# Performance work log

Hardware: AMD Instinct MI355X
Metric: run time of the kernel (lower is better)

The kernel has to match this reference:

```python
import jax, jax.numpy as jnp
import numpy as np

N_NODES = 100000
N_EDGES = 2500000
IN_CH = 32
HID = 16
OUT_CH = 32


def setup_inputs() -> dict:
    key = jax.random.key(0)
    ks = jax.random.split(key, 10)
    x = jax.random.normal(ks[0], (N_NODES, IN_CH), dtype=jnp.float32)
    edge_index = jax.random.randint(ks[1], (2, N_EDGES), 0, N_NODES, dtype=jnp.int64)
    # conv1 MLP: Linear(in,16) -> ReLU -> Linear(16,out)
    W1 = jax.random.normal(ks[2], (IN_CH, HID), dtype=jnp.float32) / np.sqrt(IN_CH)
    b1 = jnp.zeros((HID,), dtype=jnp.float32)
    W2 = jax.random.normal(ks[3], (HID, OUT_CH), dtype=jnp.float32) / np.sqrt(HID)
    b2 = jnp.zeros((OUT_CH,), dtype=jnp.float32)
    # conv2 MLP: Linear(out,16) -> ReLU -> Linear(16,out)
    W3 = jax.random.normal(ks[4], (OUT_CH, HID), dtype=jnp.float32) / np.sqrt(OUT_CH)
    b3 = jnp.zeros((HID,), dtype=jnp.float32)
    W4 = jax.random.normal(ks[5], (HID, OUT_CH), dtype=jnp.float32) / np.sqrt(HID)
    b4 = jnp.zeros((OUT_CH,), dtype=jnp.float32)
    return {"x": x, "edge_index": edge_index, "W1": W1, "b1": b1, "W2": W2,
            "b2": b2, "W3": W3, "b3": b3, "W4": W4, "b4": b4}


def _gin_conv(x, src, dst, W_a, b_a, W_b, b_b):
    # GINConv (eps=0): nn((1+eps)*x + sum_{j in N(i)} x_j)
    agg = jax.ops.segment_sum(x[src], dst, num_segments=x.shape[0])  # [N, d]
    h = x + agg
    h = jnp.maximum(h @ W_a + b_a, 0.0)  # Linear -> ReLU
    return h @ W_b + b_b                 # Linear


def reference(x, edge_index, W1, b1, W2, b2, W3, b3, W4, b4):
    src, dst = edge_index[0], edge_index[1]
    h = _gin_conv(x, src, dst, W1, b1, W2, b2)
    h = jnp.maximum(h, 0.0)  # F.relu between convs
    out = _gin_conv(h, src, dst, W3, b3, W4, b4)
    return out
```

## Files before the change

### kernel.cpp

```cpp
#include <hip/hip_runtime.h>

typedef unsigned short ushort_t;
typedef unsigned int uint_t;

#define BKT_SHIFT 8
#define BKT_NODES 256
#define NBKT_MAX 400
#define EPB 8192
#define SCOL_CAP 8192
#define NPB 32
#define SCOL_N 1536

__device__ __forceinline__ ushort_t f2bf(float f) {
    unsigned u = __float_as_uint(f);
    unsigned r = (u + 0x7FFFu + ((u >> 16) & 1u)) >> 16;
    return (ushort_t)r;
}
__device__ __forceinline__ float bflo(uint_t u) { return __uint_as_float(u << 16); }
__device__ __forceinline__ float bfhi(uint_t u) { return __uint_as_float(u & 0xFFFF0000u); }

__global__ void to_bf16(const float4* __restrict__ in, ushort_t* __restrict__ out, int n4) {
    int i = blockIdx.x * blockDim.x + threadIdx.x;
    if (i < n4) {
        float4 v = in[i];
        out[i * 4 + 0] = f2bf(v.x);
        out[i * 4 + 1] = f2bf(v.y);
        out[i * 4 + 2] = f2bf(v.z);
        out[i * 4 + 3] = f2bf(v.w);
    }
}


__global__ void histA(const int* __restrict__ dst, int* __restrict__ hist,
                      int E, int NBKT) {
    __shared__ int lcnt[NBKT_MAX];
    int t = threadIdx.x, blk = blockIdx.x;
    for (int b = t; b < NBKT; b += 512) lcnt[b] = 0;
    __syncthreads();
    int e0 = blk * EPB;
    #pragma unroll
    for (int i = 0; i < 16; ++i) {
        int e = e0 + i * 512 + t;
        if (e < E) atomicAdd(&lcnt[dst[e] >> BKT_SHIFT], 1);
    }
    __syncthreads();
    for (int b = t; b < NBKT; b += 512) hist[blk * NBKT + b] = lcnt[b];
}

__global__ void colscan(int* __restrict__ hist, int* __restrict__ T,
                        int NBLK, int NBKT) {
    __shared__ int lds[256];
    int b = blockIdx.x, t = threadIdx.x;
    int j0 = t * 4;
    int v0 = (j0 + 0 < NBLK) ? hist[(j0 + 0) * NBKT + b] : 0;
    int v1 = (j0 + 1 < NBLK) ? hist[(j0 + 1) * NBKT + b] : 0;
    int v2 = (j0 + 2 < NBLK) ? hist[(j0 + 2) * NBKT + b] : 0;
    int v3 = (j0 + 3 < NBLK) ? hist[(j0 + 3) * NBKT + b] : 0;
    lds[t] = v0 + v1 + v2 + v3;
    __syncthreads();
    for (int off = 1; off < 256; off <<= 1) {
        int add = (t >= off) ? lds[t - off] : 0;
        __syncthreads();
        lds[t] += add;
        __syncthreads();
    }
    int p = (t == 0) ? 0 : lds[t - 1];
    if (j0 + 0 < NBLK) hist[(j0 + 0) * NBKT + b] = p;  p += v0;
    if (j0 + 1 < NBLK) hist[(j0 + 1) * NBKT + b] = p;  p += v1;
    if (j0 + 2 < NBLK) hist[(j0 + 2) * NBKT + b] = p;  p += v2;
    if (j0 + 3 < NBLK) hist[(j0 + 3) * NBKT + b] = p;
    if (t == 255) T[b] = lds[255];
}

__global__ void scan_small(const int* __restrict__ in, int* __restrict__ out,
                           int M, int E) {
    __shared__ int lds[1024];
    int t = threadIdx.x;
    int base = t * 4;
    int v0 = (base + 0 < M) ? in[base + 0] : 0;
    int v1 = (base + 1 < M) ? in[base + 1] : 0;
    int v2 = (base + 2 < M) ? in[base + 2] : 0;
    int v3 = (base + 3 < M) ? in[base + 3] : 0;
    lds[t] = v0 + v1 + v2 + v3;
    __syncthreads();
    for (int off = 1; off < 1024; off <<= 1) {
        int add = (t >= off) ? lds[t - off] : 0;
        __syncthreads();
        lds[t] += add;
        __syncthreads();
    }
    int p = (t == 0) ? 0 : lds[t - 1];
    if (base + 0 < M) out[base + 0] = p;  p += v0;
    if (base + 1 < M) out[base + 1] = p;  p += v1;
    if (base + 2 < M) out[base + 2] = p;  p += v2;
    if (base + 3 < M) out[base + 3] = p;
    if (t == 0) out[M] = E;
}

__global__ void scatter_kernel(const int* __restrict__ src, const int* __restrict__ dst,
                               const int* __restrict__ hist, const int* __restrict__ Tscan,
                               int* __restrict__ staged, int E, int NBKT) {
    __shared__ int lbase[NBKT_MAX];
    __shared__ int lcur[NBKT_MAX];
    int t = threadIdx.x, blk = blockIdx.x;
    for (int b = t; b < NBKT; b += 512) {
        lbase[b] = hist[blk * NBKT + b] + Tscan[b];
        lcur[b] = 0;
    }
    __syncthreads();
    int e0 = blk * EPB;
    #pragma unroll
    for (int i = 0; i < 16; ++i) {
        int e = e0 + i * 512 + t;
        if (e < E) {
            int d = dst[e], s = src[e];
            int b = d >> BKT_SHIFT;
            int r = atomicAdd(&lcur[b], 1);
            staged[lbase[b] + r] = ((d & (BKT_NODES - 1)) << 24) | s;
        }
    }
}

__global__ void fine_fill(const int* __restrict__ staged, const int* __restrict__ Tscan,
                          int* __restrict__ rp, int* __restrict__ col,
                          int N, int E, int NBKT, int q1, int q2, int q3) {
    __shared__ int scnt[1024];
    __shared__ int srel[1024];
    __shared__ int scur[1024];
    __shared__ int swsum[256];
    __shared__ int scol[SCOL_CAP];
    int b = blockIdx.x, t = threadIdx.x;
    int n0 = b << BKT_SHIFT;
    int nn = min(BKT_NODES, N - n0);
    int e0 = Tscan[b];
    int e1 = Tscan[b + 1];
    int m = e1 - e0;

    #pragma unroll
    for (int j = 0; j < 4; ++j) { scnt[t * 4 + j] = 0; scur[t * 4 + j] = 0; }
    __syncthreads();
    for (int i = t; i < m; i += 256) {
        int v = staged[e0 + i];
        int dl = ((unsigned)v) >> 24;
        int s = v & 0xFFFFFF;
        int q = (s >= q2) ? ((s >= q3) ? 3 : 2) : ((s >= q1) ? 1 : 0);
        atomicAdd(&scnt[dl * 4 + q], 1);
    }
    __syncthreads();
    int c0 = scnt[t * 4 + 0], c1 = scnt[t * 4 + 1];
    int c2 = scnt[t * 4 + 2], c3 = scnt[t * 4 + 3];
    int tot = c0 + c1 + c2 + c3;
    swsum[t] = tot;
    __syncthreads();
    for (int off = 1; off < 256; off <<= 1) {
        int add = (t >= off) ? swsum[t - off] : 0;
        __syncthreads();
        swsum[t] += add;
        __syncthreads();
    }
    int excl = swsum[t] - tot;
    srel[t * 4 + 0] = excl;
    srel[t * 4 + 1] = excl + c0;
    srel[t * 4 + 2] = excl + c0 + c1;
    srel[t * 4 + 3] = excl + c0 + c1 + c2;
    if (t < nn) rp[n0 + t] = e0 + excl;
    if (b == NBKT - 1 && t == 0) rp[N] = E;
    __syncthreads();

    if (m <= SCOL_CAP) {
        for (int i = t; i < m; i += 256) {
            int v = staged[e0 + i];
            int dl = ((unsigned)v) >> 24;
            int s = v & 0xFFFFFF;
            int q = (s >= q2) ? ((s >= q3) ? 3 : 2) : ((s >= q1) ? 1 : 0);
            int p = srel[dl * 4 + q] + atomicAdd(&scur[dl * 4 + q], 1);
            scol[p] = s;
        }
        __syncthreads();
        for (int i = t; i < m; i += 256) col[e0 + i] = scol[i];
    } else {
        for (int i = t; i < m; i += 256) {
            int v = staged[e0 + i];
            int dl = ((unsigned)v) >> 24;
            int s = v & 0xFFFFFF;
            int q = (s >= q2) ? ((s >= q3) ? 3 : 2) : ((s >= q1) ? 1 : 0);
            int p = srel[dl * 4 + q] + atomicAdd(&scur[dl * 4 + q], 1);
            col[e0 + p] = s;
        }
    }
}


template <bool RELU_OUT, bool OUT_BF16>
__global__ void agg_mlp(const ushort_t* __restrict__ xin, const int* __restrict__ rp,
                        const int* __restrict__ col,
                        const float* __restrict__ Wa, const float* __restrict__ ba,
                        const float* __restrict__ Wb, const float* __restrict__ bb,
                        void* __restrict__ outv, int N) {
    __shared__ float sWa[32 * 16];
    __shared__ float sWb[16 * 32];
    __shared__ float sba[16], sbb[32];
    __shared__ float sv[NPB * 33];
    __shared__ float st1[NPB * 17];
    __shared__ int scol[SCOL_N];

    int t = threadIdx.x;
    sWa[t] = Wa[t];  sWa[t + 256] = Wa[t + 256];
    sWb[t] = Wb[t];  sWb[t + 256] = Wb[t + 256];
    if (t < 16) sba[t] = ba[t];
    if (t < 32) sbb[t] = bb[t];

    int base = blockIdx.x * NPB;
    int kb = rp[base];
    int kt = rp[min(base + NPB, N)];
    int tot = kt - kb;
    bool ovf = (tot > SCOL_N);
    if (!ovf) {
        for (int i = t; i < tot; i += 256)
            scol[i] = __builtin_nontemporal_load(col + kb + i);
    }
    __syncthreads();

    int ln = t >> 3;
    int sl = t & 7;
    int n  = base + ln;
    bool act = (n < N);
    const uint2* x2 = (const uint2*)xin;

    if (act) {
        uint2 us = x2[(size_t)n * 8 + sl];
        float v0 = bflo(us.x), v1 = bfhi(us.x), v2 = bflo(us.y), v3 = bfhi(us.y);
        int ks = rp[n], ke = rp[n + 1];
        if (!ovf) {
            int k = ks - kb, kend = ke - kb;
            for (; k + 8 <= kend; k += 8) {
                int s0 = scol[k + 0], s1 = scol[k + 1], s2 = scol[k + 2], s3 = scol[k + 3];
                int s4 = scol[k + 4], s5 = scol[k + 5], s6 = scol[k + 6], s7 = scol[k + 7];
                uint2 u0 = x2[(size_t)s0 * 8 + sl];
                uint2 u1 = x2[(size_t)s1 * 8 + sl];
                uint2 u2 = x2[(size_t)s2 * 8 + sl];
                uint2 u3 = x2[(size_t)s3 * 8 + sl];
                uint2 u4 = x2[(size_t)s4 * 8 + sl];
                uint2 u5 = x2[(size_t)s5 * 8 + sl];
                uint2 u6 = x2[(size_t)s6 * 8 + sl];
                uint2 u7 = x2[(size_t)s7 * 8 + sl];
                v0 += ((bflo(u0.x) + bflo(u1.x)) + (bflo(u2.x) + bflo(u3.x)))
                    + ((bflo(u4.x) + bflo(u5.x)) + (bflo(u6.x) + bflo(u7.x)));
                v1 += ((bfhi(u0.x) + bfhi(u1.x)) + (bfhi(u2.x) + bfhi(u3.x)))
                    + ((bfhi(u4.x) + bfhi(u5.x)) + (bfhi(u6.x) + bfhi(u7.x)));
                v2 += ((bflo(u0.y) + bflo(u1.y)) + (bflo(u2.y) + bflo(u3.y)))
                    + ((bflo(u4.y) + bflo(u5.y)) + (bflo(u6.y) + bflo(u7.y)));
                v3 += ((bfhi(u0.y) + bfhi(u1.y)) + (bfhi(u2.y) + bfhi(u3.y)))
                    + ((bfhi(u4.y) + bfhi(u5.y)) + (bfhi(u6.y) + bfhi(u7.y)));
            }
            for (; k < kend; ++k) {
                uint2 u = x2[(size_t)scol[k] * 8 + sl];
                v0 += bflo(u.x); v1 += bfhi(u.x); v2 += bflo(u.y); v3 += bfhi(u.y);
            }
        } else {
            for (int k = ks; k < ke; ++k) {
                uint2 u = x2[(size_t)col[k] * 8 + sl];
                v0 += bflo(u.x); v1 += bfhi(u.x); v2 += bflo(u.y); v3 += bfhi(u.y);
            }
        }
        int c0 = sl * 4;
        sv[ln * 33 + c0 + 0] = v0; sv[ln * 33 + c0 + 1] = v1;
        sv[ln * 33 + c0 + 2] = v2; sv[ln * 33 + c0 + 3] = v3;
    }
    __syncthreads();

    if (act) {
        float ha = sba[sl], hb = sba[sl + 8];
        #pragma unroll
        for (int cc = 0; cc < 32; ++cc) {
            float vc = sv[ln * 33 + cc];
            ha += vc * sWa[cc * 16 + sl];
            hb += vc * sWa[cc * 16 + sl + 8];
        }
        st1[ln * 17 + sl]     = fmaxf(ha, 0.f);
        st1[ln * 17 + sl + 8] = fmaxf(hb, 0.f);
    }
    __syncthreads();

    if (act) {
        int c0 = sl * 4;
        float a0 = sbb[c0], a1 = sbb[c0 + 1], a2 = sbb[c0 + 2], a3 = sbb[c0 + 3];
        #pragma unroll
        for (int j = 0; j < 16; ++j) {
            float hj = st1[ln * 17 + j];
            a0 += hj * sWb[j * 32 + c0];
            a1 += hj * sWb[j * 32 + c0 + 1];
            a2 += hj * sWb[j * 32 + c0 + 2];
            a3 += hj * sWb[j * 32 + c0 + 3];
        }
        if (RELU_OUT) {
            a0 = fmaxf(a0, 0.f); a1 = fmaxf(a1, 0.f);
            a2 = fmaxf(a2, 0.f); a3 = fmaxf(a3, 0.f);
        }
        if (OUT_BF16) {
            uint_t p0 = (uint_t)f2bf(a0) | ((uint_t)f2bf(a1) << 16);
            uint_t p1 = (uint_t)f2bf(a2) | ((uint_t)f2bf(a3) << 16);
            uint_t* o = (uint_t*)outv + (size_t)n * 16 + sl * 2;
            __builtin_nontemporal_store(p0, o);
            __builtin_nontemporal_store(p1, o + 1);
        } else {
            float* o = (float*)outv + (size_t)n * 32 + c0;
            __builtin_nontemporal_store(a0, o);
            __builtin_nontemporal_store(a1, o + 1);
            __builtin_nontemporal_store(a2, o + 2);
            __builtin_nontemporal_store(a3, o + 3);
        }
    }
}


extern "C" void kernel_launch(void* const* d_in, const int* in_sizes, int n_in,
                              void* d_out, int out_size, void* d_ws, size_t ws_size,
                              hipStream_t stream) {
    const float* x  = (const float*)d_in[0];
    const int*   ei = (const int*)d_in[1];
    const float* W1 = (const float*)d_in[2];
    const float* b1 = (const float*)d_in[3];
    const float* W2 = (const float*)d_in[4];
    const float* b2 = (const float*)d_in[5];
    const float* W3 = (const float*)d_in[6];
    const float* b3 = (const float*)d_in[7];
    const float* W4 = (const float*)d_in[8];
    const float* b4 = (const float*)d_in[9];

    const int N = in_sizes[0] / 32;
    const int E = in_sizes[1] / 2;
    const int* src = ei;
    const int* dst = ei + E;

    const int NBKT = (N + BKT_NODES - 1) >> BKT_SHIFT;
    const int NBLK = (E + EPB - 1) / EPB;

    char* ws = (char*)d_ws;
    size_t o = 0;
    auto alloc = [&](size_t bytes) -> char* {
        o = (o + 255) & ~(size_t)255;
        char* r = ws + o;
        o += bytes;
        return r;
    };
    int*      hist   = (int*)     alloc(4 * (size_t)NBLK * NBKT);
    int*      T      = (int*)     alloc(4 * (size_t)NBKT);
    int*      Tscan  = (int*)     alloc(4 * (size_t)(NBKT + 1));
    int*      staged = (int*)     alloc(4 * (size_t)E);
    int*      rp     = (int*)     alloc(4 * (size_t)(N + 1));
    int*      col    = (int*)     alloc(4 * (size_t)E);
    ushort_t* xb     = (ushort_t*)alloc(2 * (size_t)N * 32);
    ushort_t* hb     = (ushort_t*)alloc(2 * (size_t)N * 32);

    int n4 = N * 32 / 4;
    to_bf16<<<(n4 + 255) / 256, 256, 0, stream>>>((const float4*)x, xb, n4);

    histA<<<NBLK, 512, 0, stream>>>(dst, hist, E, NBKT);
    colscan<<<NBKT, 256, 0, stream>>>(hist, T, NBLK, NBKT);
    scan_small<<<1, 1024, 0, stream>>>(T, Tscan, NBKT, E);
    scatter_kernel<<<NBLK, 512, 0, stream>>>(src, dst, hist, Tscan, staged, E, NBKT);
    int q1 = N / 4, q2 = N / 2, q3 = (3 * N) / 4;
    fine_fill<<<NBKT, 256, 0, stream>>>(staged, Tscan, rp, col, N, E, NBKT, q1, q2, q3);

    agg_mlp<true,  true ><<<(N + NPB - 1) / NPB, 256, 0, stream>>>(xb, rp, col,
                                                                   W1, b1, W2, b2, hb, N);
    agg_mlp<false, false><<<(N + NPB - 1) / NPB, 256, 0, stream>>>(hb, rp, col,
                                                                   W3, b3, W4, b4, d_out, N);
}
```

Measured before the change: 205.2 us.

## Apply first linear before aggregation to gather 16-wide features instead of 32

```diff
diff --git a/kernel.cpp b/kernel.cpp
--- a/kernel.cpp
+++ b/kernel.cpp
@@ -8,8 +8,8 @@
 #define NBKT_MAX 400
 #define EPB 8192
 #define SCOL_CAP 8192
-#define NPB 32
-#define SCOL_N 1536
+#define NPB16 64
+#define SCOL_N16 2560
 
 __device__ __forceinline__ ushort_t f2bf(float f) {
     unsigned u = __float_as_uint(f);
@@ -19,15 +19,39 @@
 __device__ __forceinline__ float bflo(uint_t u) { return __uint_as_float(u << 16); }
 __device__ __forceinline__ float bfhi(uint_t u) { return __uint_as_float(u & 0xFFFF0000u); }
 
-__global__ void to_bf16(const float4* __restrict__ in, ushort_t* __restrict__ out, int n4) {
-    int i = blockIdx.x * blockDim.x + threadIdx.x;
-    if (i < n4) {
-        float4 v = in[i];
-        out[i * 4 + 0] = f2bf(v.x);
-        out[i * 4 + 1] = f2bf(v.y);
-        out[i * 4 + 2] = f2bf(v.z);
-        out[i * 4 + 3] = f2bf(v.w);
-    }
+__global__ void lin_in(const float4* __restrict__ x4, const float* __restrict__ W,
+                       ushort_t* __restrict__ z, int N) {
+    __shared__ float sW[32 * 16];
+    int t = threadIdx.x;
+    sW[t] = W[t];
+    sW[t + 256] = W[t + 256];
+    __syncthreads();
+    int n = blockIdx.x * 256 + t;
+    if (n >= N) return;
+    float acc[16];
+    #pragma unroll
+    for (int c = 0; c < 16; ++c) acc[c] = 0.f;
+    const float4* xr = x4 + (size_t)n * 8;
+    #pragma unroll
+    for (int k4 = 0; k4 < 8; ++k4) {
+        float4 xv = xr[k4];
+        #pragma unroll
+        for (int c = 0; c < 16; ++c) {
+            acc[c] += xv.x * sW[(k4 * 4 + 0) * 16 + c];
+            acc[c] += xv.y * sW[(k4 * 4 + 1) * 16 + c];
+            acc[c] += xv.z * sW[(k4 * 4 + 2) * 16 + c];
+            acc[c] += xv.w * sW[(k4 * 4 + 3) * 16 + c];
+        }
+    }
+    uint_t w[8];
+    #pragma unroll
+    for (int i = 0; i < 8; ++i)
+        w[i] = (uint_t)f2bf(acc[2 * i]) | ((uint_t)f2bf(acc[2 * i + 1]) << 16);
+    uint4* zo = (uint4*)(z + (size_t)n * 16);
+    uint4 a; a.x = w[0]; a.y = w[1]; a.z = w[2]; a.w = w[3];
+    uint4 b; b.x = w[4]; b.y = w[5]; b.z = w[6]; b.w = w[7];
+    zo[0] = a;
+    zo[1] = b;
 }
 
 
@@ -191,44 +215,45 @@
 }
 
 
-template <bool RELU_OUT, bool OUT_BF16>
-__global__ void agg_mlp(const ushort_t* __restrict__ xin, const int* __restrict__ rp,
-                        const int* __restrict__ col,
-                        const float* __restrict__ Wa, const float* __restrict__ ba,
-                        const float* __restrict__ Wb, const float* __restrict__ bb,
-                        void* __restrict__ outv, int N) {
-    __shared__ float sWa[32 * 16];
+template <bool CHAIN>
+__global__ void agg_mlp16(const ushort_t* __restrict__ zin, const int* __restrict__ rp,
+                          const int* __restrict__ col,
+                          const float* __restrict__ ba,
+                          const float* __restrict__ Wb, const float* __restrict__ bb,
+                          const float* __restrict__ Wc,
+                          void* __restrict__ outv, int N) {
     __shared__ float sWb[16 * 32];
+    __shared__ float sWc[32 * 16];
     __shared__ float sba[16], sbb[32];
-    __shared__ float sv[NPB * 33];
-    __shared__ float st1[NPB * 17];
-    __shared__ int scol[SCOL_N];
+    __shared__ float sh[NPB16 * 17];
+    __shared__ float sr[NPB16 * 33];
+    __shared__ int scol[SCOL_N16];
 
     int t = threadIdx.x;
-    sWa[t] = Wa[t];  sWa[t + 256] = Wa[t + 256];
     sWb[t] = Wb[t];  sWb[t + 256] = Wb[t + 256];
+    if (CHAIN) { sWc[t] = Wc[t];  sWc[t + 256] = Wc[t + 256]; }
     if (t < 16) sba[t] = ba[t];
     if (t < 32) sbb[t] = bb[t];
 
-    int base = blockIdx.x * NPB;
+    int base = blockIdx.x * NPB16;
     int kb = rp[base];
-    int kt = rp[min(base + NPB, N)];
+    int kt = rp[min(base + NPB16, N)];
     int tot = kt - kb;
-    bool ovf = (tot > SCOL_N);
+    bool ovf = (tot > SCOL_N16);
     if (!ovf) {
         for (int i = t; i < tot; i += 256)
             scol[i] = __builtin_nontemporal_load(col + kb + i);
     }
     __syncthreads();
 
-    int ln = t >> 3;
-    int sl = t & 7;
+    int ln = t >> 2;
+    int sl = t & 3;
     int n  = base + ln;
     bool act = (n < N);
-    const uint2* x2 = (const uint2*)xin;
+    const uint2* zp = (const uint2*)zin;
 
     if (act) {
-        uint2 us = x2[(size_t)n * 8 + sl];
+        uint2 us = zp[(size_t)n * 4 + sl];
         float v0 = bflo(us.x), v1 = bfhi(us.x), v2 = bflo(us.y), v3 = bfhi(us.y);
         int ks = rp[n], ke = rp[n + 1];
         if (!ovf) {
@@ -236,14 +261,14 @@
             for (; k + 8 <= kend; k += 8) {
                 int s0 = scol[k + 0], s1 = scol[k + 1], s2 = scol[k + 2], s3 = scol[k + 3];
                 int s4 = scol[k + 4], s5 = scol[k + 5], s6 = scol[k + 6], s7 = scol[k + 7];
-                uint2 u0 = x2[(size_t)s0 * 8 + sl];
-                uint2 u1 = x2[(size_t)s1 * 8 + sl];
-                uint2 u2 = x2[(size_t)s2 * 8 + sl];
-                uint2 u3 = x2[(size_t)s3 * 8 + sl];
-                uint2 u4 = x2[(size_t)s4 * 8 + sl];
-                uint2 u5 = x2[(size_t)s5 * 8 + sl];
-                uint2 u6 = x2[(size_t)s6 * 8 + sl];
-                uint2 u7 = x2[(size_t)s7 * 8 + sl];
+                uint2 u0 = zp[(size_t)s0 * 4 + sl];
+                uint2 u1 = zp[(size_t)s1 * 4 + sl];
+                uint2 u2 = zp[(size_t)s2 * 4 + sl];
+                uint2 u3 = zp[(size_t)s3 * 4 + sl];
+                uint2 u4 = zp[(size_t)s4 * 4 + sl];
+                uint2 u5 = zp[(size_t)s5 * 4 + sl];
+                uint2 u6 = zp[(size_t)s6 * 4 + sl];
+                uint2 u7 = zp[(size_t)s7 * 4 + sl];
                 v0 += ((bflo(u0.x) + bflo(u1.x)) + (bflo(u2.x) + bflo(u3.x)))
                     + ((bflo(u4.x) + bflo(u5.x)) + (bflo(u6.x) + bflo(u7.x)));
                 v1 += ((bfhi(u0.x) + bfhi(u1.x)) + (bfhi(u2.x) + bfhi(u3.x)))
@@ -254,61 +279,64 @@
                     + ((bfhi(u4.y) + bfhi(u5.y)) + (bfhi(u6.y) + bfhi(u7.y)));
             }
             for (; k < kend; ++k) {
-                uint2 u = x2[(size_t)scol[k] * 8 + sl];
+                uint2 u = zp[(size_t)scol[k] * 4 + sl];
                 v0 += bflo(u.x); v1 += bfhi(u.x); v2 += bflo(u.y); v3 += bfhi(u.y);
             }
         } else {
             for (int k = ks; k < ke; ++k) {
-                uint2 u = x2[(size_t)col[k] * 8 + sl];
+                uint2 u = zp[(size_t)col[k] * 4 + sl];
                 v0 += bflo(u.x); v1 += bfhi(u.x); v2 += bflo(u.y); v3 += bfhi(u.y);
             }
         }
         int c0 = sl * 4;
-        sv[ln * 33 + c0 + 0] = v0; sv[ln * 33 + c0 + 1] = v1;
-        sv[ln * 33 + c0 + 2] = v2; sv[ln * 33 + c0 + 3] = v3;
+        sh[ln * 17 + c0 + 0] = fmaxf(v0 + sba[c0 + 0], 0.f);
+        sh[ln * 17 + c0 + 1] = fmaxf(v1 + sba[c0 + 1], 0.f);
+        sh[ln * 17 + c0 + 2] = fmaxf(v2 + sba[c0 + 2], 0.f);
+        sh[ln * 17 + c0 + 3] = fmaxf(v3 + sba[c0 + 3], 0.f);
     }
     __syncthreads();
 
     if (act) {
-        float ha = sba[sl], hb = sba[sl + 8];
+        int c0 = sl * 8;
+        float o[8];
         #pragma unroll
-        for (int cc = 0; cc < 32; ++cc) {
-            float vc = sv[ln * 33 + cc];
-            ha += vc * sWa[cc * 16 + sl];
-            hb += vc * sWa[cc * 16 + sl + 8];
-        }
-        st1[ln * 17 + sl]     = fmaxf(ha, 0.f);
-        st1[ln * 17 + sl + 8] = fmaxf(hb, 0.f);
-    }
-    __syncthreads();
-
-    if (act) {
-        int c0 = sl * 4;
-        float a0 = sbb[c0], a1 = sbb[c0 + 1], a2 = sbb[c0 + 2], a3 = sbb[c0 + 3];
+        for (int j = 0; j < 8; ++j) o[j] = sbb[c0 + j];
         #pragma unroll
         for (int j = 0; j < 16; ++j) {
-            float hj = st1[ln * 17 + j];
-            a0 += hj * sWb[j * 32 + c0];
-            a1 += hj * sWb[j * 32 + c0 + 1];
-            a2 += hj * sWb[j * 32 + c0 + 2];
-            a3 += hj * sWb[j * 32 + c0 + 3];
-        }
-        if (RELU_OUT) {
-            a0 = fmaxf(a0, 0.f); a1 = fmaxf(a1, 0.f);
-            a2 = fmaxf(a2, 0.f); a3 = fmaxf(a3, 0.f);
-        }
-        if (OUT_BF16) {
+            float hj = sh[ln * 17 + j];
+            #pragma unroll
+            for (int cc = 0; cc < 8; ++cc)
+                o[cc] += hj * sWb[j * 32 + c0 + cc];
+        }
+        if (CHAIN) {
+            #pragma unroll
+            for (int cc = 0; cc < 8; ++cc)
+                sr[ln * 33 + c0 + cc] = fmaxf(o[cc], 0.f);
+        } else {
+            float* op = (float*)outv + (size_t)n * 32 + c0;
+            #pragma unroll
+            for (int cc = 0; cc < 8; ++cc)
+                __builtin_nontemporal_store(o[cc], op + cc);
+        }
+    }
+    if (CHAIN) {
+        __syncthreads();
+        if (act) {
+            int c0 = sl * 4;
+            float a0 = 0.f, a1 = 0.f, a2 = 0.f, a3 = 0.f;
+            #pragma unroll
+            for (int j = 0; j < 32; ++j) {
+                float rj = sr[ln * 33 + j];
+                a0 += rj * sWc[j * 16 + c0 + 0];
+                a1 += rj * sWc[j * 16 + c0 + 1];
+                a2 += rj * sWc[j * 16 + c0 + 2];
+                a3 += rj * sWc[j * 16 + c0 + 3];
+            }
             uint_t p0 = (uint_t)f2bf(a0) | ((uint_t)f2bf(a1) << 16);
             uint_t p1 = (uint_t)f2bf(a2) | ((uint_t)f2bf(a3) << 16);
-            uint_t* o = (uint_t*)outv + (size_t)n * 16 + sl * 2;
-            __builtin_nontemporal_store(p0, o);
-            __builtin_nontemporal_store(p1, o + 1);
-        } else {
-            float* o = (float*)outv + (size_t)n * 32 + c0;
-            __builtin_nontemporal_store(a0, o);
-            __builtin_nontemporal_store(a1, o + 1);
-            __builtin_nontemporal_store(a2, o + 2);
-            __builtin_nontemporal_store(a3, o + 3);
+            uint_t* op = (uint_t*)outv + (size_t)n * 8 + sl * 2;
+            op[0] = p0;
+            op[1] = p1;
         }
     }
 }
@@ -350,11 +378,10 @@
     int*      staged = (int*)     alloc(4 * (size_t)E);
     int*      rp     = (int*)     alloc(4 * (size_t)(N + 1));
     int*      col    = (int*)     alloc(4 * (size_t)E);
-    ushort_t* xb     = (ushort_t*)alloc(2 * (size_t)N * 32);
-    ushort_t* hb     = (ushort_t*)alloc(2 * (size_t)N * 32);
-
-    int n4 = N * 32 / 4;
-    to_bf16<<<(n4 + 255) / 256, 256, 0, stream>>>((const float4*)x, xb, n4);
+    ushort_t* zb     = (ushort_t*)alloc(2 * (size_t)N * 16);
+    ushort_t* z2b    = (ushort_t*)alloc(2 * (size_t)N * 16);
+
+    lin_in<<<(N + 255) / 256, 256, 0, stream>>>((const float4*)x, W1, zb, N);
 
     histA<<<NBLK, 512, 0, stream>>>(dst, hist, E, NBKT);
     colscan<<<NBKT, 256, 0, stream>>>(hist, T, NBLK, NBKT);
@@ -363,8 +390,8 @@
     int q1 = N / 4, q2 = N / 2, q3 = (3 * N) / 4;
     fine_fill<<<NBKT, 256, 0, stream>>>(staged, Tscan, rp, col, N, E, NBKT, q1, q2, q3);
 
-    agg_mlp<true,  true ><<<(N + NPB - 1) / NPB, 256, 0, stream>>>(xb, rp, col,
-                                                                   W1, b1, W2, b2, hb, N);
-    agg_mlp<false, false><<<(N + NPB - 1) / NPB, 256, 0, stream>>>(hb, rp, col,
-                                                                   W3, b3, W4, b4, d_out, N);
-}
+    agg_mlp16<true ><<<(N + NPB16 - 1) / NPB16, 256, 0, stream>>>(
+        zb, rp, col, b1, W2, b2, W3, z2b, N);
+    agg_mlp16<false><<<(N + NPB16 - 1) / NPB16, 256, 0, stream>>>(
+        z2b, rp, col, b3, W4, b4, nullptr, d_out, N);
+}
```

Measured after the change: 199.9 us. -2.6%, faster.
